# Optimization experiments

Hardware: AMD Instinct MI355X
Metric: run time of the kernel (lower is better)

Reference implementation:

```python
import jax, jax.numpy as jnp
import numpy as np

N_NODES = 50000
N_EDGES = 600000
D_FEAT = 128


def setup_inputs() -> dict:
    key = jax.random.key(0)
    k_h, k_src, k_dst, k_dt, k_norm = jax.random.split(key, 5)
    h = jax.random.normal(k_h, (N_NODES, D_FEAT), dtype=jnp.float32)
    src = jax.random.randint(k_src, (N_EDGES,), 0, N_NODES, dtype=jnp.int32)
    dst = jax.random.randint(k_dst, (N_EDGES,), 0, N_NODES, dtype=jnp.int32)
    # dt: non-negative time deltas (scaled up a bit so the decay matters)
    dt = jax.random.uniform(k_dt, (N_EDGES,), dtype=jnp.float32) * 10.0
    # norm: symmetric-normalization-like positive edge weights
    norm = jax.random.uniform(k_norm, (N_EDGES,), dtype=jnp.float32)
    decay_lam = jnp.full((1,), 0.1, dtype=jnp.float32)  # nn.Parameter(0.1)
    return {"h": h, "src": src, "dst": dst, "dt": dt, "norm": norm, "decay_lam": decay_lam}


def reference(h, src, dst, dt, norm, decay_lam):
    # lam = relu(decay_lam) + 1e-4  (scalar)
    lam = jax.nn.relu(decay_lam[0]) + 1e-4
    # per-edge temporal weight: norm * exp(-lam * dt)   [E]
    w = norm * jnp.exp(-lam * dt)
    # u_mul_e: gather source features, scale by edge weight  [E, D]
    m = h[src] * w[:, None]
    # sum-reduce messages at destination nodes  [N, D]
    h_new = jax.ops.segment_sum(m, dst, num_segments=h.shape[0])
    return h_new
```

## Files before the change

kernel.cpp:

```cpp
#include <hip/hip_runtime.h>
#include <hip/hip_bf16.h>

#define D_FEAT 128
#define BIN_SHIFT 7
#define NODES_PER_BIN 128
#define BCAP 4096
#define EPB 2048
#define T1 512
#define CSR_L_CAP 5120
#define OVF_CAP 4096

typedef float f2v __attribute__((ext_vector_type(2)));

__device__ __forceinline__ unsigned bf16_rne(float f) {
    unsigned u = __float_as_uint(f);
    return (u + 0x7fffu + ((u >> 16) & 1u)) >> 16;
}

__global__ void __launch_bounds__(T1)
conv_bin_kernel(const float* __restrict__ h,
                const int* __restrict__ src, const int* __restrict__ dst,
                const float* __restrict__ dt, const float* __restrict__ norm,
                const float* __restrict__ decay_lam,
                unsigned* __restrict__ hb,
                int* __restrict__ bin_cursor, unsigned long long* __restrict__ binned,
                int* __restrict__ ovf_cnt, int* __restrict__ ovf_d,
                int* __restrict__ ovf_s, float* __restrict__ ovf_w,
                int E, int HN4, int convBlocks, int NB) {
    __shared__ unsigned hist[T1];
    __shared__ unsigned cur[T1];
    __shared__ unsigned gbase[T1];

    int t = threadIdx.x;
    if (blockIdx.x < convBlocks) {
        int i = blockIdx.x * T1 + t;
        if (i < HN4) {
            float4 v = ((const float4*)h)[i];
            ((uint2*)hb)[i] = make_uint2(bf16_rne(v.x) | (bf16_rne(v.y) << 16),
                                         bf16_rne(v.z) | (bf16_rne(v.w) << 16));
        }
        return;
    }

    int e0 = (blockIdx.x - convBlocks) * EPB;

    hist[t] = 0; cur[t] = 0;
    __syncthreads();

    float lam = fmaxf(decay_lam[0], 0.0f) + 1e-4f;

    unsigned long long ent[EPB / T1];
    int bn[EPB / T1];
    #pragma unroll
    for (int k = 0; k < EPB / T1; ++k) {
        int e = e0 + k * T1 + t;
        bn[k] = -1;
        if (e < E) {
            int s = src[e], d = dst[e];
            float w = norm[e] * expf(-lam * dt[e]);
            int b = d >> BIN_SHIFT;
            int l = d & (NODES_PER_BIN - 1);
            ent[k] = ((unsigned long long)l << 32) | (((unsigned)s << 16) | bf16_rne(w));
            bn[k] = b;
            atomicAdd(&hist[b], 1u);
        }
    }
    __syncthreads();

    if (t < NB && hist[t] > 0)
        gbase[t] = (unsigned)atomicAdd(&bin_cursor[t], (int)hist[t]);
    __syncthreads();

    #pragma unroll
    for (int k = 0; k < EPB / T1; ++k) {
        if (bn[k] >= 0) {
            int b = bn[k];
            unsigned gp = gbase[b] + atomicAdd(&cur[b], 1u);
            if (gp < BCAP) {
                binned[(size_t)b * BCAP + gp] = ent[k];
            } else {
                int o = atomicAdd(ovf_cnt, 1);
                if (o < OVF_CAP) {
                    int l = (int)(ent[k] >> 32);
                    ovf_d[o] = (b << BIN_SHIFT) | l;
                    ovf_s[o] = (int)((ent[k] >> 16) & 0xFFFFu);
                    ovf_w[o] = __uint_as_float(((unsigned)ent[k] & 0xFFFFu) << 16);
                }
            }
        }
    }
}

__global__ void __launch_bounds__(T1)
sort_gather_kernel(const unsigned long long* __restrict__ binned,
                   const int* __restrict__ bin_cursor,
                   const unsigned* __restrict__ hb,
                   const int* __restrict__ ovf_cnt, const int* __restrict__ ovf_d,
                   const int* __restrict__ ovf_s, const float* __restrict__ ovf_w,
                   float* __restrict__ out, int N) {
    __shared__ unsigned hist[NODES_PER_BIN];
    __shared__ unsigned padoff[NODES_PER_BIN];
    __shared__ unsigned cur[NODES_PER_BIN];
    __shared__ unsigned csr_l[CSR_L_CAP];
    __shared__ unsigned wtot;

    int b = blockIdx.x;
    int t = threadIdx.x;
    int cnt = min(bin_cursor[b], BCAP);

    if (t < NODES_PER_BIN) { hist[t] = 0; cur[t] = 0; }
    for (int i = t; i < CSR_L_CAP; i += T1) csr_l[i] = 0;
    __syncthreads();

    unsigned long long ent[BCAP / T1];
    size_t base_in = (size_t)b * BCAP;
    #pragma unroll
    for (int k = 0; k < BCAP / T1; ++k) {
        int idx = k * T1 + t;
        ent[k] = ~0ull;
        if (idx < cnt) {
            unsigned long long e = binned[base_in + idx];
            ent[k] = e;
            atomicAdd(&hist[(int)(e >> 32)], 1u);
        }
    }
    __syncthreads();

    unsigned pc = 0, val = 0;
    if (t < NODES_PER_BIN) { pc = (hist[t] + 7u) & ~7u; val = pc; }
    #pragma unroll
    for (int off = 1; off < 64; off <<= 1) {
        unsigned u = __shfl_up(val, off, 64);
        if ((t & 63) >= off) val += u;
    }
    if (t == 63) wtot = val;
    __syncthreads();
    if (t < NODES_PER_BIN)
        padoff[t] = val + ((t >= 64) ? wtot : 0u) - pc;
    __syncthreads();

    #pragma unroll
    for (int k = 0; k < BCAP / T1; ++k) {
        if (ent[k] != ~0ull) {
            int l = (int)(ent[k] >> 32);
            unsigned p = padoff[l] + atomicAdd(&cur[l], 1u);
            csr_l[p] = (unsigned)ent[k];
        }
    }
    __syncthreads();

    int wid = t >> 6;
    int lane = t & 63;
    int nodes = min(NODES_PER_BIN, N - (b << BIN_SHIFT));
    bool ovf_bin = bin_cursor[b] > BCAP;

    for (int l = wid; l < nodes; l += 8) {
        unsigned base = padoff[l];
        unsigned mr = (hist[l] + 7u) & ~7u;
        float accx = 0.0f, accy = 0.0f;
        for (unsigned j = 0; j < mr; j += 8) {
            unsigned u0 = csr_l[base + j + 0];
            unsigned u1 = csr_l[base + j + 1];
            unsigned u2 = csr_l[base + j + 2];
            unsigned u3 = csr_l[base + j + 3];
            unsigned u4 = csr_l[base + j + 4];
            unsigned u5 = csr_l[base + j + 5];
            unsigned u6 = csr_l[base + j + 6];
            unsigned u7 = csr_l[base + j + 7];
            unsigned v0 = hb[(size_t)(u0 >> 16) * 64 + lane];
            unsigned v1 = hb[(size_t)(u1 >> 16) * 64 + lane];
            unsigned v2 = hb[(size_t)(u2 >> 16) * 64 + lane];
            unsigned v3 = hb[(size_t)(u3 >> 16) * 64 + lane];
            unsigned v4 = hb[(size_t)(u4 >> 16) * 64 + lane];
            unsigned v5 = hb[(size_t)(u5 >> 16) * 64 + lane];
            unsigned v6 = hb[(size_t)(u6 >> 16) * 64 + lane];
            unsigned v7 = hb[(size_t)(u7 >> 16) * 64 + lane];
            #define ACC(u, v)                                             \
            {   float wf = __uint_as_float((u) << 16);                    \
                float vx = __uint_as_float((v) << 16);                    \
                float vy = __uint_as_float((v) & 0xffff0000u);            \
                accx += vx * wf; accy += vy * wf; }
            ACC(u0, v0) ACC(u1, v1) ACC(u2, v2) ACC(u3, v3)
            ACC(u4, v4) ACC(u5, v5) ACC(u6, v6) ACC(u7, v7)
            #undef ACC
        }
        int node = (b << BIN_SHIFT) + l;
        if (ovf_bin) {
            int oc = min(*ovf_cnt, OVF_CAP);
            for (int o = 0; o < oc; ++o) {
                if (ovf_d[o] == node) {
                    float we = ovf_w[o];
                    unsigned v = hb[(size_t)ovf_s[o] * 64 + lane];
                    accx += __uint_as_float(v << 16) * we;
                    accy += __uint_as_float(v & 0xffff0000u) * we;
                }
            }
        }
        f2v r;
        r.x = accx; r.y = accy;
        __builtin_nontemporal_store(r, (f2v*)(out + (size_t)node * D_FEAT) + lane);
    }
}


__global__ void degree_kernel(const int* __restrict__ dst, int* __restrict__ deg, int E) {
    int e = blockIdx.x * blockDim.x + threadIdx.x;
    if (e >= E) return;
    atomicAdd(&deg[dst[e]], 1);
}

__global__ void scan_blocks(const int* __restrict__ deg, int* __restrict__ offs,
                            int* __restrict__ blockSums, int N) {
    __shared__ int tmp[256];
    int tid = threadIdx.x;
    int gid = blockIdx.x * 256 + tid;
    int v = (gid < N) ? deg[gid] : 0;
    tmp[tid] = v;
    __syncthreads();
    for (int off = 1; off < 256; off <<= 1) {
        int t = (tid >= off) ? tmp[tid - off] : 0;
        __syncthreads();
        tmp[tid] += t;
        __syncthreads();
    }
    if (gid < N) offs[gid] = tmp[tid] - v;
    if (tid == 255) blockSums[blockIdx.x] = tmp[255];
}

__global__ void scan_sums(int* __restrict__ blockSums, int* __restrict__ blockOffs, int nb) {
    __shared__ int tmp[256];
    int tid = threadIdx.x;
    int v = (tid < nb) ? blockSums[tid] : 0;
    tmp[tid] = v;
    __syncthreads();
    for (int off = 1; off < 256; off <<= 1) {
        int t = (tid >= off) ? tmp[tid - off] : 0;
        __syncthreads();
        tmp[tid] += t;
        __syncthreads();
    }
    if (tid < nb) blockOffs[tid] = tmp[tid] - v;
}

__global__ void scan_fixup(int* __restrict__ offs, const int* __restrict__ blockOffs,
                           int* __restrict__ cursor, int N) {
    int gid = blockIdx.x * 256 + threadIdx.x;
    if (gid >= N) return;
    int o = offs[gid] + blockOffs[blockIdx.x];
    offs[gid] = o;
    cursor[gid] = o;
}

__global__ void bucket_kernel(const int* __restrict__ src, const int* __restrict__ dst,
                              const float* __restrict__ dt, const float* __restrict__ norm,
                              const float* __restrict__ decay_lam,
                              int* __restrict__ cursor, float2* __restrict__ pairs, int E) {
    int e = blockIdx.x * blockDim.x + threadIdx.x;
    if (e >= E) return;
    float lam = fmaxf(decay_lam[0], 0.0f) + 1e-4f;
    float w = norm[e] * expf(-lam * dt[e]);
    int d = dst[e];
    int pos = atomicAdd(&cursor[d], 1);
    float2 p;
    p.x = __int_as_float(src[e]);
    p.y = w;
    pairs[pos] = p;
}

__global__ void __launch_bounds__(256)
gather_kernel(const float* __restrict__ h,
              const int* __restrict__ offs, const int* __restrict__ deg,
              const float2* __restrict__ pairs, float* __restrict__ out, int N) {
    int node = blockIdx.x * 4 + (threadIdx.x >> 6);
    if (node >= N) return;
    int lane = threadIdx.x & 63;
    int start = offs[node];
    int end = start + deg[node];
    float accx = 0.0f, accy = 0.0f;
    for (int j = start; j < end; ++j) {
        float2 p = pairs[j];
        int s = __float_as_int(p.x);
        float we = p.y;
        float2 v = ((const float2*)(h + (size_t)s * D_FEAT))[lane];
        accx += v.x * we;
        accy += v.y * we;
    }
    float2 r; r.x = accx; r.y = accy;
    ((float2*)(out + (size_t)node * D_FEAT))[lane] = r;
}

extern "C" void kernel_launch(void* const* d_in, const int* in_sizes, int n_in,
                              void* d_out, int out_size, void* d_ws, size_t ws_size,
                              hipStream_t stream) {
    const float* h         = (const float*)d_in[0];
    const int*   src       = (const int*)d_in[1];
    const int*   dst       = (const int*)d_in[2];
    const float* dt        = (const float*)d_in[3];
    const float* norm      = (const float*)d_in[4];
    const float* decay_lam = (const float*)d_in[5];
    float* out = (float*)d_out;

    const int E  = in_sizes[1];
    const int HN = in_sizes[0];
    const int N  = out_size / D_FEAT;
    const int NB = (N + NODES_PER_BIN - 1) >> BIN_SHIFT;

    auto align64 = [](size_t x) { return (x + 63) & ~(size_t)63; };
    size_t sz_binc = align64((size_t)NB * 4);
    size_t sz_ovfc = 64;
    size_t sz_ovf  = align64((size_t)OVF_CAP * 4);
    size_t sz_binn = align64((size_t)NB * BCAP * 8);
    size_t sz_hb   = align64((size_t)HN * 2);
    size_t need = sz_binc + sz_ovfc + 3 * sz_ovf + sz_binn + sz_hb;

    if (ws_size >= need && N <= 65536 && (HN & 3) == 0 && NB <= T1) {
        char* ws = (char*)d_ws;
        int* bin_cursor = (int*)ws;                 ws += sz_binc;
        int* ovf_cnt    = (int*)ws;                 ws += sz_ovfc;
        int* ovf_d      = (int*)ws;                 ws += sz_ovf;
        int* ovf_s      = (int*)ws;                 ws += sz_ovf;
        float* ovf_w    = (float*)ws;               ws += sz_ovf;
        unsigned long long* binned = (unsigned long long*)ws;  ws += sz_binn;
        unsigned* hb    = (unsigned*)ws;

        hipMemsetAsync(bin_cursor, 0, sz_binc + sz_ovfc, stream);

        const int HN4 = HN / 4;
        const int convBlocks = (HN4 + T1 - 1) / T1;
        const int binBlocks  = (E + EPB - 1) / EPB;
        conv_bin_kernel<<<convBlocks + binBlocks, T1, 0, stream>>>(
            h, src, dst, dt, norm, decay_lam, hb, bin_cursor, binned,
            ovf_cnt, ovf_d, ovf_s, ovf_w, E, HN4, convBlocks, NB);

        sort_gather_kernel<<<NB, T1, 0, stream>>>(
            binned, bin_cursor, hb, ovf_cnt, ovf_d, ovf_s, ovf_w, out, N);
    } else {
        const int nb = (N + 255) / 256;
        char* ws = (char*)d_ws;
        int*    dega      = (int*)ws;     ws += (size_t)N * 4;
        int*    offsa     = (int*)ws;     ws += (size_t)N * 4;
        int*    cursor    = (int*)ws;     ws += (size_t)N * 4;
        int*    blockSums = (int*)ws;     ws += 256 * 4;
        int*    blockOffs = (int*)ws;     ws += 256 * 4;
        float2* pairs     = (float2*)ws;

        hipMemsetAsync(dega, 0, (size_t)N * 4, stream);
        degree_kernel<<<(E + 255) / 256, 256, 0, stream>>>(dst, dega, E);
        scan_blocks<<<nb, 256, 0, stream>>>(dega, offsa, blockSums, N);
        scan_sums<<<1, 256, 0, stream>>>(blockSums, blockOffs, nb);
        scan_fixup<<<nb, 256, 0, stream>>>(offsa, blockOffs, cursor, N);
        bucket_kernel<<<(E + 255) / 256, 256, 0, stream>>>(
            src, dst, dt, norm, decay_lam, cursor, pairs, E);
        gather_kernel<<<(N + 3) / 4, 256, 0, stream>>>(h, offsa, dega, pairs, out, N);
    }
}
```

Baseline: 127.2 us.

## Replace global bin cursors with per-block fixed-capacity sub-bins

The binning stage no longer takes a global atomic per bin. Each edge block instead writes into its own fixed 32-slot sub-bucket per destination bin and records a per-(bin, block) count. The sort stage then scans all sub-buckets of its bin, reading each bin's entries twice from global memory instead of holding them in registers. This removes the block-wide histogram pass and the contended global atomics, at the cost of many sparse, partially filled slots that must be traversed. Overflow handling now fires whenever any sub-bucket overflows, and with about 10 edges per block per bin that should rarely happen.

```diff
diff --git a/kernel.cpp b/kernel.cpp
--- a/kernel.cpp
+++ b/kernel.cpp
@@ -4,9 +4,10 @@
 #define D_FEAT 128
 #define BIN_SHIFT 7
 #define NODES_PER_BIN 128
-#define BCAP 4096
+#define CAP_BB 32
 #define EPB 2048
 #define T1 512
+#define NBLK_MAX 512
 #define CSR_L_CAP 5120
 #define OVF_CAP 4096
 
@@ -23,13 +24,11 @@
                 const float* __restrict__ dt, const float* __restrict__ norm,
                 const float* __restrict__ decay_lam,
                 unsigned* __restrict__ hb,
-                int* __restrict__ bin_cursor, unsigned long long* __restrict__ binned,
+                int* __restrict__ cnt_g, unsigned long long* __restrict__ binned,
                 int* __restrict__ ovf_cnt, int* __restrict__ ovf_d,
                 int* __restrict__ ovf_s, float* __restrict__ ovf_w,
-                int E, int HN4, int convBlocks, int NB) {
-    __shared__ unsigned hist[T1];
+                int E, int HN4, int convBlocks, int NB, int nblk) {
     __shared__ unsigned cur[T1];
-    __shared__ unsigned gbase[T1];
 
     int t = threadIdx.x;
     if (blockIdx.x < convBlocks) {
@@ -42,85 +41,69 @@
         return;
     }
 
-    int e0 = (blockIdx.x - convBlocks) * EPB;
-
-    hist[t] = 0; cur[t] = 0;
+    int blk = blockIdx.x - convBlocks;
+    int e0 = blk * EPB;
+
+    cur[t] = 0;
     __syncthreads();
 
     float lam = fmaxf(decay_lam[0], 0.0f) + 1e-4f;
 
-    unsigned long long ent[EPB / T1];
-    int bn[EPB / T1];
     #pragma unroll
     for (int k = 0; k < EPB / T1; ++k) {
         int e = e0 + k * T1 + t;
-        bn[k] = -1;
         if (e < E) {
             int s = src[e], d = dst[e];
             float w = norm[e] * expf(-lam * dt[e]);
             int b = d >> BIN_SHIFT;
             int l = d & (NODES_PER_BIN - 1);
-            ent[k] = ((unsigned long long)l << 32) | (((unsigned)s << 16) | bf16_rne(w));
-            bn[k] = b;
-            atomicAdd(&hist[b], 1u);
-        }
-    }
-    __syncthreads();
-
-    if (t < NB && hist[t] > 0)
-        gbase[t] = (unsigned)atomicAdd(&bin_cursor[t], (int)hist[t]);
-    __syncthreads();
-
-    #pragma unroll
-    for (int k = 0; k < EPB / T1; ++k) {
-        if (bn[k] >= 0) {
-            int b = bn[k];
-            unsigned gp = gbase[b] + atomicAdd(&cur[b], 1u);
-            if (gp < BCAP) {
-                binned[(size_t)b * BCAP + gp] = ent[k];
+            unsigned long long ent =
+                ((unsigned long long)l << 32) | (((unsigned)s << 16) | bf16_rne(w));
+            unsigned i = atomicAdd(&cur[b], 1u);
+            if (i < CAP_BB) {
+                binned[((size_t)b * nblk + blk) * CAP_BB + i] = ent;
             } else {
                 int o = atomicAdd(ovf_cnt, 1);
                 if (o < OVF_CAP) {
-                    int l = (int)(ent[k] >> 32);
                     ovf_d[o] = (b << BIN_SHIFT) | l;
-                    ovf_s[o] = (int)((ent[k] >> 16) & 0xFFFFu);
-                    ovf_w[o] = __uint_as_float(((unsigned)ent[k] & 0xFFFFu) << 16);
+                    ovf_s[o] = s;
+                    ovf_w[o] = __uint_as_float((unsigned)(ent & 0xFFFFu) << 16);
                 }
             }
         }
     }
+    __syncthreads();
+    if (t < NB) cnt_g[(size_t)t * nblk + blk] = (int)min(cur[t], (unsigned)CAP_BB);
 }
 
 __global__ void __launch_bounds__(T1)
 sort_gather_kernel(const unsigned long long* __restrict__ binned,
-                   const int* __restrict__ bin_cursor,
+                   const int* __restrict__ cnt_g,
                    const unsigned* __restrict__ hb,
                    const int* __restrict__ ovf_cnt, const int* __restrict__ ovf_d,
                    const int* __restrict__ ovf_s, const float* __restrict__ ovf_w,
-                   float* __restrict__ out, int N) {
+                   float* __restrict__ out, int N, int nblk) {
     __shared__ unsigned hist[NODES_PER_BIN];
     __shared__ unsigned padoff[NODES_PER_BIN];
     __shared__ unsigned cur[NODES_PER_BIN];
     __shared__ unsigned csr_l[CSR_L_CAP];
+    __shared__ unsigned cntl[NBLK_MAX];
     __shared__ unsigned wtot;
 
     int b = blockIdx.x;
     int t = threadIdx.x;
-    int cnt = min(bin_cursor[b], BCAP);
+    size_t rbase = (size_t)b * nblk * CAP_BB;
 
     if (t < NODES_PER_BIN) { hist[t] = 0; cur[t] = 0; }
     for (int i = t; i < CSR_L_CAP; i += T1) csr_l[i] = 0;
-    __syncthreads();
-
-    unsigned long long ent[BCAP / T1];
-    size_t base_in = (size_t)b * BCAP;
-    #pragma unroll
-    for (int k = 0; k < BCAP / T1; ++k) {
-        int idx = k * T1 + t;
-        ent[k] = ~0ull;
-        if (idx < cnt) {
-            unsigned long long e = binned[base_in + idx];
-            ent[k] = e;
+    for (int i = t; i < nblk; i += T1) cntl[i] = (unsigned)cnt_g[(size_t)b * nblk + i];
+    __syncthreads();
+
+    int total_slots = nblk * CAP_BB;
+
+    for (int s = t; s < total_slots; s += T1) {
+        if ((unsigned)(s & (CAP_BB - 1)) < cntl[s / CAP_BB]) {
+            unsigned long long e = binned[rbase + s];
             atomicAdd(&hist[(int)(e >> 32)], 1u);
         }
     }
@@ -139,12 +122,12 @@
         padoff[t] = val + ((t >= 64) ? wtot : 0u) - pc;
     __syncthreads();
 
-    #pragma unroll
-    for (int k = 0; k < BCAP / T1; ++k) {
-        if (ent[k] != ~0ull) {
-            int l = (int)(ent[k] >> 32);
+    for (int s = t; s < total_slots; s += T1) {
+        if ((unsigned)(s & (CAP_BB - 1)) < cntl[s / CAP_BB]) {
+            unsigned long long e = binned[rbase + s];
+            int l = (int)(e >> 32);
             unsigned p = padoff[l] + atomicAdd(&cur[l], 1u);
-            csr_l[p] = (unsigned)ent[k];
+            if (p < CSR_L_CAP) csr_l[p] = (unsigned)e;
         }
     }
     __syncthreads();
@@ -152,11 +135,13 @@
     int wid = t >> 6;
     int lane = t & 63;
     int nodes = min(NODES_PER_BIN, N - (b << BIN_SHIFT));
-    bool ovf_bin = bin_cursor[b] > BCAP;
+    bool ovf_any = (*ovf_cnt) > 0;
 
     for (int l = wid; l < nodes; l += 8) {
         unsigned base = padoff[l];
+        if (base >= CSR_L_CAP) continue;
         unsigned mr = (hist[l] + 7u) & ~7u;
+        if (base + mr > CSR_L_CAP) mr = (CSR_L_CAP - base) & ~7u;
         float accx = 0.0f, accy = 0.0f;
         for (unsigned j = 0; j < mr; j += 8) {
             unsigned u0 = csr_l[base + j + 0];
@@ -185,7 +170,7 @@
             #undef ACC
         }
         int node = (b << BIN_SHIFT) + l;
-        if (ovf_bin) {
+        if (ovf_any) {
             int oc = min(*ovf_cnt, OVF_CAP);
             for (int o = 0; o < oc; ++o) {
                 if (ovf_d[o] == node) {
@@ -304,36 +289,37 @@
     const int HN = in_sizes[0];
     const int N  = out_size / D_FEAT;
     const int NB = (N + NODES_PER_BIN - 1) >> BIN_SHIFT;
+    const int nblk = (E + EPB - 1) / EPB;
 
     auto align64 = [](size_t x) { return (x + 63) & ~(size_t)63; };
-    size_t sz_binc = align64((size_t)NB * 4);
     size_t sz_ovfc = 64;
     size_t sz_ovf  = align64((size_t)OVF_CAP * 4);
-    size_t sz_binn = align64((size_t)NB * BCAP * 8);
+    size_t sz_cnt  = align64((size_t)NB * nblk * 4);
+    size_t sz_binn = align64((size_t)NB * nblk * CAP_BB * 8);
     size_t sz_hb   = align64((size_t)HN * 2);
-    size_t need = sz_binc + sz_ovfc + 3 * sz_ovf + sz_binn + sz_hb;
-
-    if (ws_size >= need && N <= 65536 && (HN & 3) == 0 && NB <= T1) {
+    size_t need = sz_ovfc + 3 * sz_ovf + sz_cnt + sz_binn + sz_hb;
+
+    if (ws_size >= need && N <= 65536 && (HN & 3) == 0 &&
+        NB <= T1 && nblk <= NBLK_MAX) {
         char* ws = (char*)d_ws;
-        int* bin_cursor = (int*)ws;                 ws += sz_binc;
         int* ovf_cnt    = (int*)ws;                 ws += sz_ovfc;
         int* ovf_d      = (int*)ws;                 ws += sz_ovf;
         int* ovf_s      = (int*)ws;                 ws += sz_ovf;
         float* ovf_w    = (float*)ws;               ws += sz_ovf;
+        int* cnt_g      = (int*)ws;                 ws += sz_cnt;
         unsigned long long* binned = (unsigned long long*)ws;  ws += sz_binn;
         unsigned* hb    = (unsigned*)ws;
 
-        hipMemsetAsync(bin_cursor, 0, sz_binc + sz_ovfc, stream);
+        hipMemsetAsync(ovf_cnt, 0, sz_ovfc, stream);
 
         const int HN4 = HN / 4;
         const int convBlocks = (HN4 + T1 - 1) / T1;
-        const int binBlocks  = (E + EPB - 1) / EPB;
-        conv_bin_kernel<<<convBlocks + binBlocks, T1, 0, stream>>>(
-            h, src, dst, dt, norm, decay_lam, hb, bin_cursor, binned,
-            ovf_cnt, ovf_d, ovf_s, ovf_w, E, HN4, convBlocks, NB);
+        conv_bin_kernel<<<convBlocks + nblk, T1, 0, stream>>>(
+            h, src, dst, dt, norm, decay_lam, hb, cnt_g, binned,
+            ovf_cnt, ovf_d, ovf_s, ovf_w, E, HN4, convBlocks, NB, nblk);
 
         sort_gather_kernel<<<NB, T1, 0, stream>>>(
-            binned, bin_cursor, hb, ovf_cnt, ovf_d, ovf_s, ovf_w, out, N);
+            binned, cnt_g, hb, ovf_cnt, ovf_d, ovf_s, ovf_w, out, N, nblk);
     } else {
         const int nb = (N + 255) / 256;
         char* ws = (char*)d_ws;
```

New measurement: 148.8 us. 17.0% more time.
